# Performance work log

Hardware: AMD Instinct MI355X
Metric: run time of the kernel (lower is better)

Reference implementation:

```python
import jax, jax.numpy as jnp
import numpy as np
from jax import lax

L, H, NUM_CONVS, KSIZE = 8192, 128, 4, 7
EPS = 1e-5


def _pos_encoding(length, dim, dtype):
    pos = jnp.arange(length, dtype=jnp.float32)[:, None]
    i = jnp.arange(dim, dtype=jnp.float32)[None, :]
    angle = pos / jnp.power(10000.0, (2.0 * jnp.floor(i / 2.0)) / dim)
    pe = jnp.where((jnp.arange(dim) % 2 == 0)[None, :], jnp.sin(angle), jnp.cos(angle))
    return pe.astype(dtype)


def _layer_norm(x):
    mu = jnp.mean(x, axis=-1, keepdims=True)
    var = jnp.mean(jnp.square(x - mu), axis=-1, keepdims=True)
    return (x - mu) * lax.rsqrt(var + EPS)


def _conv1d_same(x, w, b):
    # x: [L, H]; w: [H_out, H_in, K]; b: [H_out]. SAME padding over sequence.
    lhs = x.T[None]  # [1, H, L]
    out = lax.conv_general_dilated(lhs, w, window_strides=(1,), padding='SAME',
                                   dimension_numbers=('NCH', 'OIH', 'NCH'))
    return (out[0] + b[:, None]).T  # [L, H]


def setup_inputs() -> dict:
    key = jax.random.key(0)
    ks = jax.random.split(key, 12)
    s = 0.02
    return {
        'x': jax.random.normal(ks[0], (L, H), jnp.float32),
        'conv_w': jax.random.normal(ks[1], (NUM_CONVS, H, H, KSIZE), jnp.float32) * s,
        'conv_b': jax.random.normal(ks[2], (NUM_CONVS, H), jnp.float32) * s,
        'Wq': jax.random.normal(ks[3], (H, H), jnp.float32) * s,
        'bq': jax.random.normal(ks[4], (H,), jnp.float32) * s,
        'Wk': jax.random.normal(ks[5], (H, H), jnp.float32) * s,
        'bk': jax.random.normal(ks[6], (H,), jnp.float32) * s,
        'Wv': jax.random.normal(ks[7], (H, H), jnp.float32) * s,
        'bv': jax.random.normal(ks[8], (H,), jnp.float32) * s,
        'Wff': jax.random.normal(ks[9], (H, H), jnp.float32) * s,
        'bff': jax.random.normal(ks[10], (H,), jnp.float32) * s,
    }


def reference(x, conv_w, conv_b, Wq, bq, Wk, bk, Wv, bv, Wff, bff):
    h = x + _pos_encoding(x.shape[0], x.shape[1], x.dtype)
    # conv stack: LN -> conv -> residual, repeated num_convs times
    for i in range(NUM_CONVS):
        residual = h
        h = _conv1d_same(_layer_norm(h), conv_w[i], conv_b[i]) + residual
    # self-attention (single-head as written in the source)
    residual = h
    n = _layer_norm(h)
    q = n @ Wq.T + bq
    k = n @ Wk.T + bk
    v = n @ Wv.T + bv
    scale = 1.0 / jnp.sqrt(jnp.asarray(H, h.dtype))
    attn = jax.nn.softmax((q @ k.T) * scale, axis=-1)  # [L, L]
    h = attn @ v + residual
    # feed-forward
    residual = h
    h = jax.nn.relu(_layer_norm(h) @ Wff.T + bff) + residual
    return h
```

## Files before the change

kernel.cpp:

```cpp
#include <hip/hip_runtime.h>

#define LL 8192
#define HH 128

typedef __attribute__((ext_vector_type(8))) short short8v;
typedef __attribute__((ext_vector_type(4))) short short4v;
typedef __attribute__((ext_vector_type(4))) float f32x4;

__device__ inline short f2bf(float f) {
    union { float f; unsigned u; } x; x.f = f;
    unsigned r = (x.u + 0x7fffu + ((x.u >> 16) & 1u)) >> 16;
    return (short)r;
}
__device__ inline float bf2f(short s) {
    union { unsigned u; float f; } x; x.u = ((unsigned)(unsigned short)s) << 16;
    return x.f;
}

__device__ inline short* sAp(short* base, int row, int col) {
    int byte = (row << 8) + (col << 1);
    byte ^= (row & 7) << 4;
    return (short*)((char*)base + byte);
}

__device__ inline short8v ln_pack8(const float* rowF, int l15) {
    const float4 a = *(const float4*)&rowF[l15 * 8];
    const float4 b = *(const float4*)&rowF[l15 * 8 + 4];
    float s  = (a.x + a.y) + (a.z + a.w) + (b.x + b.y) + (b.z + b.w);
    float s2 = a.x * a.x + a.y * a.y + a.z * a.z + a.w * a.w
             + b.x * b.x + b.y * b.y + b.z * b.z + b.w * b.w;
#pragma unroll
    for (int off = 1; off <= 8; off <<= 1) {
        s  += __shfl_xor(s,  off, 64);
        s2 += __shfl_xor(s2, off, 64);
    }
    float mu = s * (1.f / 128.f);
    float var = s2 * (1.f / 128.f) - mu * mu;
    float rstd = rsqrtf(var + 1e-5f);
    short8v r;
    r[0] = f2bf((a.x - mu) * rstd);
    r[1] = f2bf((a.y - mu) * rstd);
    r[2] = f2bf((a.z - mu) * rstd);
    r[3] = f2bf((a.w - mu) * rstd);
    r[4] = f2bf((b.x - mu) * rstd);
    r[5] = f2bf((b.y - mu) * rstd);
    r[6] = f2bf((b.z - mu) * rstd);
    r[7] = f2bf((b.w - mu) * rstd);
    return r;
}

__global__ __launch_bounds__(256) void repack_all(const float* __restrict__ x,
                                                  const float* __restrict__ w,
                                                  const float* __restrict__ Wq,
                                                  const float* __restrict__ Wk,
                                                  const float* __restrict__ Wv,
                                                  const float* __restrict__ bq,
                                                  const float* __restrict__ bk,
                                                  const float* __restrict__ bv,
                                                  const float* __restrict__ Wff,
                                                  short* __restrict__ wkb,
                                                  short* __restrict__ wqkvb,
                                                  float* __restrict__ b3,
                                                  short* __restrict__ wffb,
                                                  float* __restrict__ h0) {
    const float qs = 0.08838834764831845f;
    int idx = blockIdx.x * 256 + threadIdx.x;
    if (idx < 458752) {
        int k = idx % 7;
        int t = idx / 7;
        int i = t % HH; t /= HH;
        int o = t % HH;
        int lay = t / HH;
        wkb[((lay * 7 + k) * HH + o) * HH + i] = f2bf(w[idx]);
    } else {
        int j = idx - 458752;
        if (j < 49152) {
            int t = j >> 14, r = j & 16383;
            float v = (t == 0) ? Wq[r] * qs : (t == 1) ? Wk[r] : Wv[r];
            wqkvb[j] = f2bf(v);
        } else if (j < 49536) {
            int jj = j - 49152;
            b3[jj] = (jj < 128) ? bq[jj] * qs : (jj < 256) ? bk[jj - 128] : bv[jj - 256];
        } else if (j < 65920) {
            int jj = j - 49536;
            wffb[jj] = f2bf(Wff[jj]);
        } else {
            int p = j - 65920;
            if (p < 262144) {
                int g = p >> 5, c4 = (p & 31) << 2;
                float4 val = *(const float4*)&x[g * HH + c4];
                float fg = (float)g;
#pragma unroll
                for (int h = 0; h < 2; h++) {
                    int i0 = c4 + h * 2;
                    float e = (float)i0 / 128.f;
                    float ang = fg / powf(10000.f, e);
                    ((float*)&val)[h * 2]     += sinf(ang);
                    ((float*)&val)[h * 2 + 1] += cosf(ang);
                }
                *(float4*)&h0[g * HH + c4] = val;
            }
        }
    }
}

__global__ __launch_bounds__(256, 4) void conv4qkv_kernel(const float* __restrict__ h0,
                                                          const short* __restrict__ wkb,
                                                          const float* __restrict__ conv_b,
                                                          const short* __restrict__ wqkvb,
                                                          const float* __restrict__ b3,
                                                          float* __restrict__ hB,
                                                          short* __restrict__ qb,
                                                          short* __restrict__ kb,
                                                          short* __restrict__ vt) {
    __shared__ float sF[48][132];
    __shared__ short sA[54 * 128];
    short* sT = sA + 20 * 128;
    int tid = threadIdx.x;
    int w = tid >> 6, lane = tid & 63;
    int l15 = lane & 15, quad = lane >> 4;
    int m0 = blockIdx.x * 16;
    int c0 = w * 32;

    for (int idx = tid; idx < 48 * 32; idx += 256) {
        int r = idx >> 5, c4 = (idx & 31) << 2;
        int g = m0 - 16 + r;
        float4 val = make_float4(0.f, 0.f, 0.f, 0.f);
        if (g >= 0 && g < LL) val = *(const float4*)&h0[g * HH + c4];
        *(float4*)&sF[r][c4] = val;
    }
    for (int idx = tid; idx < 6 * 64; idx += 256) {
        int rr = idx >> 6, cc = idx & 63;
        int row = (rr < 3) ? rr : 48 + rr;
        ((unsigned*)sA)[row * 64 + cc] = 0u;
    }

    for (int lay = 0; lay < 4; lay++) {
        __syncthreads();
#pragma unroll
        for (int rr = 0; rr < 3; rr++) {
            int row = rr * 16 + w * 4 + quad;
            short8v pk = ln_pack8(&sF[row][0], l15);
            int g = m0 - 16 + row;
            if (g < 0 || g >= LL) pk = (short8v)(short)0;
            *(short8v*)sAp(sA, row + 3, l15 * 8) = pk;
        }
        __syncthreads();
        f32x4 acc[3][2];
#pragma unroll
        for (int mt = 0; mt < 3; mt++) { acc[mt][0] = (f32x4)(0.f); acc[mt][1] = (f32x4)(0.f); }
        const short* wl = wkb + lay * 7 * HH * HH;
        for (int k = 0; k < 7; k++) {
            const short* b0 = wl + (k * HH + c0 + l15) * HH;
            const short* b1 = b0 + 16 * HH;
#pragma unroll
            for (int ks = 0; ks < 4; ks++) {
                short8v bf0 = *(const short8v*)&b0[ks * 32 + quad * 8];
                short8v bf1 = *(const short8v*)&b1[ks * 32 + quad * 8];
#pragma unroll
                for (int mt = 0; mt < 3; mt++) {
                    short8v af = *(const short8v*)sAp(sA, mt * 16 + l15 + k, ks * 32 + quad * 8);
                    acc[mt][0] = __builtin_amdgcn_mfma_f32_16x16x32_bf16(af, bf0, acc[mt][0], 0, 0, 0);
                    acc[mt][1] = __builtin_amdgcn_mfma_f32_16x16x32_bf16(af, bf1, acc[mt][1], 0, 0, 0);
                }
            }
        }
        float bb0 = conv_b[lay * HH + c0 + l15], bb1 = conv_b[lay * HH + c0 + 16 + l15];
#pragma unroll
        for (int mt = 0; mt < 3; mt++)
#pragma unroll
            for (int r = 0; r < 4; r++) {
                int row = mt * 16 + quad * 4 + r;
                sF[row][c0 + l15]      += acc[mt][0][r] + bb0;
                sF[row][c0 + 16 + l15] += acc[mt][1][r] + bb1;
            }
    }
    __syncthreads();
    for (int idx = tid; idx < 16 * 32; idx += 256) {
        int r = idx >> 5, c4 = (idx & 31) << 2;
        *(float4*)&hB[(m0 + r) * HH + c4] = *(const float4*)&sF[16 + r][c4];
    }
    {
        int row = w * 4 + quad;
        *(short8v*)sAp(sA, row, l15 * 8) = ln_pack8(&sF[16 + row][0], l15);
    }
    __syncthreads();
    short8v af4[4];
#pragma unroll
    for (int ks = 0; ks < 4; ks++)
        af4[ks] = *(const short8v*)sAp(sA, l15, ks * 32 + quad * 8);

    for (int t = 0; t < 3; t++) {
        f32x4 acc0 = (f32x4)(0.f), acc1 = (f32x4)(0.f);
        const short* b0 = wqkvb + (t * 128 + c0 + l15) * HH;
        const short* b1 = b0 + 16 * HH;
#pragma unroll
        for (int ks = 0; ks < 4; ks++) {
            short8v bf0 = *(const short8v*)&b0[ks * 32 + quad * 8];
            short8v bf1 = *(const short8v*)&b1[ks * 32 + quad * 8];
            acc0 = __builtin_amdgcn_mfma_f32_16x16x32_bf16(af4[ks], bf0, acc0, 0, 0, 0);
            acc1 = __builtin_amdgcn_mfma_f32_16x16x32_bf16(af4[ks], bf1, acc1, 0, 0, 0);
        }
        float bb0 = b3[t * 128 + c0 + l15], bb1 = b3[t * 128 + c0 + 16 + l15];
        if (t < 2) {
            short* o = (t == 0) ? qb : kb;
#pragma unroll
            for (int r = 0; r < 4; r++) {
                int lr = m0 + quad * 4 + r;
                o[lr * HH + c0 + l15]      = f2bf(acc0[r] + bb0);
                o[lr * HH + c0 + 16 + l15] = f2bf(acc1[r] + bb1);
            }
        } else {
#pragma unroll
            for (int r = 0; r < 4; r++) {
                sT[(w * 32 + l15) * 17 + quad * 4 + r]      = f2bf(acc0[r] + bb0);
                sT[(w * 32 + 16 + l15) * 17 + quad * 4 + r] = f2bf(acc1[r] + bb1);
            }
            asm volatile("s_waitcnt lgkmcnt(0)" ::: "memory");
#pragma unroll
            for (int cc = 0; cc < 8; cc++) {
                int col = cc * 4 + quad;
                vt[(c0 + col) * LL + m0 + l15] = sT[(w * 32 + col) * 17 + l15];
            }
        }
    }
}

#define FBN 64

__global__ __launch_bounds__(256, 2) void flash_mfma_kernel(const short* __restrict__ qs,
                                                            const short* __restrict__ ksrc,
                                                            const short* __restrict__ vsrc,
                                                            short* __restrict__ PO,
                                                            float* __restrict__ Pl,
                                                            int segrows) {
    __shared__ short sK[16 * 64 * 8];
    __shared__ short sV[16 * 64 * 8];
    __shared__ short sP[4][32][72];

    const int tid = threadIdx.x;
    const int w = tid >> 6, lane = tid & 63;
    const int l15 = lane & 15, quad = lane >> 4;
    const int m0 = blockIdx.x * 128;
    const int seg = blockIdx.y;
    const int jbeg = seg * segrows;
    const int nchunk = segrows >> 6;

    const int vdt_base = (w >> 1);
    const int vks2 = w & 1;

    short8v qf[2][4];
#pragma unroll
    for (int mt = 0; mt < 2; mt++)
#pragma unroll
        for (int ks = 0; ks < 4; ks++)
            qf[mt][ks] = *(const short8v*)&qs[(m0 + w * 32 + mt * 16 + l15) * HH + ks * 32 + quad * 8];

    float l_r[2][4] = {{0.f, 0.f, 0.f, 0.f}, {0.f, 0.f, 0.f, 0.f}};
    f32x4 o_acc[2][8];
#pragma unroll
    for (int mt = 0; mt < 2; mt++)
#pragma unroll
        for (int dt = 0; dt < 8; dt++) o_acc[mt][dt] = (f32x4)(0.f);

    short8v kr[4], vr[4];
#pragma unroll
    for (int r = 0; r < 4; r++) {
        kr[r] = *(const short8v*)&ksrc[(jbeg + r * 16 + l15) * HH + w * 32 + quad * 8];
        vr[r] = *(const short8v*)&vsrc[((2 * r + vdt_base) * 16 + l15) * LL + jbeg + vks2 * 32 + quad * 8];
    }

    for (int c = 0; c < nchunk; c++) {
        __syncthreads();
#pragma unroll
        for (int r = 0; r < 4; r++) {
            *(short8v*)&sK[((w + 4 * r) * 64 + lane) * 8] = kr[r];
            *(short8v*)&sV[((w + 4 * r) * 64 + lane) * 8] = vr[r];
        }
        __syncthreads();
        if (c + 1 < nchunk) {
            const int j1 = jbeg + (c + 1) * FBN;
#pragma unroll
            for (int r = 0; r < 4; r++) {
                kr[r] = *(const short8v*)&ksrc[(j1 + r * 16 + l15) * HH + w * 32 + quad * 8];
                vr[r] = *(const short8v*)&vsrc[((2 * r + vdt_base) * 16 + l15) * LL + j1 + vks2 * 32 + quad * 8];
            }
        }
        f32x4 s_acc[2][4];
#pragma unroll
        for (int mt = 0; mt < 2; mt++)
#pragma unroll
            for (int nt = 0; nt < 4; nt++) s_acc[mt][nt] = (f32x4)(0.f);
#pragma unroll
        for (int nt = 0; nt < 4; nt++)
#pragma unroll
            for (int ks = 0; ks < 4; ks++) {
                short8v kf = *(const short8v*)&sK[((nt * 4 + ks) * 64 + lane) * 8];
                s_acc[0][nt] = __builtin_amdgcn_mfma_f32_16x16x32_bf16(qf[0][ks], kf, s_acc[0][nt], 0, 0, 0);
                s_acc[1][nt] = __builtin_amdgcn_mfma_f32_16x16x32_bf16(qf[1][ks], kf, s_acc[1][nt], 0, 0, 0);
            }
#pragma unroll
        for (int mt = 0; mt < 2; mt++)
#pragma unroll
            for (int nt = 0; nt < 4; nt++)
#pragma unroll
                for (int r = 0; r < 4; r++) {
                    float p = __expf(fminf(s_acc[mt][nt][r], 30.f));
                    l_r[mt][r] += p;
                    union { float f; unsigned u; } cv; cv.f = p;
                    sP[w][mt * 16 + quad * 4 + r][nt * 16 + l15] = (short)(cv.u >> 16);
                }
        asm volatile("s_waitcnt lgkmcnt(0)" ::: "memory");
#pragma unroll
        for (int ks2 = 0; ks2 < 2; ks2++) {
            short8v pf0 = *(const short8v*)&sP[w][l15][ks2 * 32 + quad * 8];
            short8v pf1 = *(const short8v*)&sP[w][16 + l15][ks2 * 32 + quad * 8];
#pragma unroll
            for (int dt = 0; dt < 8; dt++) {
                short8v vf = *(const short8v*)&sV[((dt * 2 + ks2) * 64 + lane) * 8];
                o_acc[0][dt] = __builtin_amdgcn_mfma_f32_16x16x32_bf16(pf0, vf, o_acc[0][dt], 0, 0, 0);
                o_acc[1][dt] = __builtin_amdgcn_mfma_f32_16x16x32_bf16(pf1, vf, o_acc[1][dt], 0, 0, 0);
            }
        }
    }
#pragma unroll
    for (int mt = 0; mt < 2; mt++)
#pragma unroll
        for (int r = 0; r < 4; r++) {
            float v = l_r[mt][r];
            v += __shfl_xor(v, 1, 64);
            v += __shfl_xor(v, 2, 64);
            v += __shfl_xor(v, 4, 64);
            v += __shfl_xor(v, 8, 64);
            if (l15 == 0)
                Pl[seg * LL + m0 + w * 32 + mt * 16 + quad * 4 + r] = v;
        }
#pragma unroll
    for (int mt = 0; mt < 2; mt++)
#pragma unroll
        for (int dt = 0; dt < 8; dt++)
#pragma unroll
            for (int r = 0; r < 4; r++)
                PO[(size_t)seg * LL * HH + (m0 + w * 32 + mt * 16 + quad * 4 + r) * HH + dt * 16 + l15] =
                    f2bf(o_acc[mt][dt][r]);
}

__global__ __launch_bounds__(256) void ff_kernel(const float* __restrict__ hin,
                                                 const short* __restrict__ PO,
                                                 const float* __restrict__ Pl,
                                                 const short* __restrict__ wffb,
                                                 const float* __restrict__ bff,
                                                 float* __restrict__ out,
                                                 int nsplit) {
    __shared__ float sF[16][132];
    __shared__ short sA[16 * 128];
    __shared__ float sLi[16];
    int tid = threadIdx.x;
    int w = tid >> 6, lane = tid & 63;
    int l15 = lane & 15, quad = lane >> 4;
    int m0 = blockIdx.x * 16;

    if (tid < 16) {
        float s = 0.f;
        for (int seg = 0; seg < nsplit; seg++) s += Pl[seg * LL + m0 + tid];
        sLi[tid] = 1.f / s;
    }
    __syncthreads();
    for (int idx = tid; idx < 16 * 32; idx += 256) {
        int r = idx >> 5, c4 = (idx & 31) << 2;
        float4 hv = *(const float4*)&hin[(m0 + r) * HH + c4];
        float s0 = 0.f, s1 = 0.f, s2 = 0.f, s3 = 0.f;
        for (int seg = 0; seg < nsplit; seg++) {
            short4v pv = *(const short4v*)&PO[(size_t)seg * LL * HH + (m0 + r) * HH + c4];
            s0 += bf2f(pv[0]); s1 += bf2f(pv[1]); s2 += bf2f(pv[2]); s3 += bf2f(pv[3]);
        }
        float li = sLi[r];
        *(float4*)&sF[r][c4] = make_float4(hv.x + s0 * li, hv.y + s1 * li,
                                           hv.z + s2 * li, hv.w + s3 * li);
    }
    __syncthreads();
    {
        int row = w * 4 + quad;
        *(short8v*)sAp(sA, row, l15 * 8) = ln_pack8(&sF[row][0], l15);
    }
    __syncthreads();
    int c0 = w * 32;
    f32x4 acc0 = (f32x4)(0.f), acc1 = (f32x4)(0.f);
    const short* b0 = wffb + (c0 + l15) * HH;
    const short* b1 = b0 + 16 * HH;
#pragma unroll
    for (int ks = 0; ks < 4; ks++) {
        short8v af = *(const short8v*)sAp(sA, l15, ks * 32 + quad * 8);
        short8v bf0 = *(const short8v*)&b0[ks * 32 + quad * 8];
        short8v bf1 = *(const short8v*)&b1[ks * 32 + quad * 8];
        acc0 = __builtin_amdgcn_mfma_f32_16x16x32_bf16(af, bf0, acc0, 0, 0, 0);
        acc1 = __builtin_amdgcn_mfma_f32_16x16x32_bf16(af, bf1, acc1, 0, 0, 0);
    }
    float bb0 = bff[c0 + l15], bb1 = bff[c0 + 16 + l15];
#pragma unroll
    for (int r = 0; r < 4; r++) {
        int lr = quad * 4 + r;
        out[(m0 + lr) * HH + c0 + l15]      = fmaxf(acc0[r] + bb0, 0.f) + sF[lr][c0 + l15];
        out[(m0 + lr) * HH + c0 + 16 + l15] = fmaxf(acc1[r] + bb1, 0.f) + sF[lr][c0 + 16 + l15];
    }
}

extern "C" void kernel_launch(void* const* d_in, const int* in_sizes, int n_in,
                              void* d_out, int out_size, void* d_ws, size_t ws_size,
                              hipStream_t stream) {
    const float* x      = (const float*)d_in[0];
    const float* conv_w = (const float*)d_in[1];
    const float* conv_b = (const float*)d_in[2];
    const float* Wq = (const float*)d_in[3];
    const float* bq = (const float*)d_in[4];
    const float* Wk = (const float*)d_in[5];
    const float* bk = (const float*)d_in[6];
    const float* Wv = (const float*)d_in[7];
    const float* bv = (const float*)d_in[8];
    const float* Wff = (const float*)d_in[9];
    const float* bff = (const float*)d_in[10];
    float* out = (float*)d_out;

    char* ws = (char*)d_ws;
    const size_t MB = 1u << 20;
    float* hB   = (float*)(ws);
    short* qb   = (short*)(ws + 4 * MB);
    short* kb   = (short*)(ws + 6 * MB);
    short* vt   = (short*)(ws + 8 * MB);
    float* Pl   = (float*)(ws + 10 * MB);
    short* wffb = (short*)(ws + 10 * MB + 524288);
    short* PO   = (short*)(ws + 10 * MB + 524288 + 32768);
    short* wkb   = (short*)(ws + 16 * MB);
    short* wqkvb = (short*)(ws + 17 * MB);
    float* b3    = (float*)(ws + 17 * MB + 131072);
    float* h0    = (float*)(ws + 18 * MB);

    int nsplit = (ws_size >= (size_t)44 * MB) ? 16 : 8;
    int segrows = LL / nsplit;

    repack_all<<<3074, 256, 0, stream>>>(x, conv_w, Wq, Wk, Wv, bq, bk, bv, Wff,
                                         wkb, wqkvb, b3, wffb, h0);
    conv4qkv_kernel<<<LL / 16, 256, 0, stream>>>(h0, wkb, conv_b, wqkvb, b3,
                                                 hB, qb, kb, vt);
    flash_mfma_kernel<<<dim3(LL / 128, nsplit), 256, 0, stream>>>(qb, kb, vt, PO, Pl, segrows);
    ff_kernel<<<LL / 16, 256, 0, stream>>>(hB, PO, Pl, wffb, bff, out, nsplit);
}
```

Before: 224.4 us.

## Split fused conv stack into per-layer kernels and separate QKV kernel

Replaces the fused conv4qkv kernel, which recomputed a 48-row halo window per 16-row tile to run all four conv layers in shared memory, with four per-layer conv launches that each need only a 3-row halo. Each layer round-trips through global memory, and the output columns are split across two blocks for more parallelism. QKV projection becomes its own kernel with a grid dimension per Q/K/V. This removes the roughly 3x redundant halo compute of the fused version. In exchange it adds extra launches and global memory traffic for the intermediate activations.

After: 229.6 us. 1.02x slower.

```diff
diff --git a/kernel.cpp b/kernel.cpp
--- a/kernel.cpp
+++ b/kernel.cpp
@@ -104,124 +104,112 @@
     }
 }
 
-__global__ __launch_bounds__(256, 4) void conv4qkv_kernel(const float* __restrict__ h0,
-                                                          const short* __restrict__ wkb,
-                                                          const float* __restrict__ conv_b,
-                                                          const short* __restrict__ wqkvb,
-                                                          const float* __restrict__ b3,
-                                                          float* __restrict__ hB,
-                                                          short* __restrict__ qb,
-                                                          short* __restrict__ kb,
-                                                          short* __restrict__ vt) {
-    __shared__ float sF[48][132];
-    __shared__ short sA[54 * 128];
-    short* sT = sA + 20 * 128;
+__global__ __launch_bounds__(256, 4) void conv_layer_kernel(const float* __restrict__ hin,
+                                                            const short* __restrict__ wkb,
+                                                            const float* __restrict__ conv_b,
+                                                            float* __restrict__ hout,
+                                                            int lay) {
+    __shared__ float sF[22][132];
+    __shared__ short sA[22 * 128];
+    int tid = threadIdx.x;
+    int w = tid >> 6, lane = tid & 63;
+    int l15 = lane & 15, quad = lane >> 4;
+    int m0 = (blockIdx.x >> 1) * 16;
+    int c0w = (blockIdx.x & 1) * 64 + w * 16;
+
+    for (int idx = tid; idx < 22 * 32; idx += 256) {
+        int r = idx >> 5, c4 = (idx & 31) << 2;
+        int g = m0 - 3 + r;
+        float4 val = make_float4(0.f, 0.f, 0.f, 0.f);
+        if (g >= 0 && g < LL) val = *(const float4*)&hin[g * HH + c4];
+        *(float4*)&sF[r][c4] = val;
+    }
+    __syncthreads();
+#pragma unroll
+    for (int rr = 0; rr < 2; rr++) {
+        int row = rr * 16 + w * 4 + quad;
+        if (row < 22)
+            *(short8v*)sAp(sA, row, l15 * 8) = ln_pack8(&sF[row][0], l15);
+    }
+    __syncthreads();
+    f32x4 accA = (f32x4)(0.f), accB = (f32x4)(0.f);
+    const short* wl = wkb + lay * 7 * HH * HH;
+    for (int k = 0; k < 7; k++) {
+        const short* b0 = wl + (k * HH + c0w + l15) * HH;
+#pragma unroll
+        for (int ks = 0; ks < 4; ks++) {
+            short8v bf = *(const short8v*)&b0[ks * 32 + quad * 8];
+            short8v af = *(const short8v*)sAp(sA, l15 + k, ks * 32 + quad * 8);
+            if (ks & 1) accB = __builtin_amdgcn_mfma_f32_16x16x32_bf16(af, bf, accB, 0, 0, 0);
+            else        accA = __builtin_amdgcn_mfma_f32_16x16x32_bf16(af, bf, accA, 0, 0, 0);
+        }
+    }
+    float bb = conv_b[lay * HH + c0w + l15];
+#pragma unroll
+    for (int r = 0; r < 4; r++) {
+        int row = quad * 4 + r;
+        hout[(m0 + row) * HH + c0w + l15] =
+            sF[3 + row][c0w + l15] + accA[r] + accB[r] + bb;
+    }
+}
+
+__global__ __launch_bounds__(256, 4) void qkv_kernel(const float* __restrict__ h4,
+                                                     const short* __restrict__ wqkvb,
+                                                     const float* __restrict__ b3,
+                                                     short* __restrict__ qb,
+                                                     short* __restrict__ kb,
+                                                     short* __restrict__ vt) {
+    __shared__ float sF[16][132];
+    __shared__ short sA[16 * 128];
+    __shared__ short sT[4][32][17];
     int tid = threadIdx.x;
     int w = tid >> 6, lane = tid & 63;
     int l15 = lane & 15, quad = lane >> 4;
     int m0 = blockIdx.x * 16;
-    int c0 = w * 32;
-
-    for (int idx = tid; idx < 48 * 32; idx += 256) {
-        int r = idx >> 5, c4 = (idx & 31) << 2;
-        int g = m0 - 16 + r;
-        float4 val = make_float4(0.f, 0.f, 0.f, 0.f);
-        if (g >= 0 && g < LL) val = *(const float4*)&h0[g * HH + c4];
-        *(float4*)&sF[r][c4] = val;
-    }
-    for (int idx = tid; idx < 6 * 64; idx += 256) {
-        int rr = idx >> 6, cc = idx & 63;
-        int row = (rr < 3) ? rr : 48 + rr;
-        ((unsigned*)sA)[row * 64 + cc] = 0u;
-    }
-
-    for (int lay = 0; lay < 4; lay++) {
-        __syncthreads();
-#pragma unroll
-        for (int rr = 0; rr < 3; rr++) {
-            int row = rr * 16 + w * 4 + quad;
-            short8v pk = ln_pack8(&sF[row][0], l15);
-            int g = m0 - 16 + row;
-            if (g < 0 || g >= LL) pk = (short8v)(short)0;
-            *(short8v*)sAp(sA, row + 3, l15 * 8) = pk;
-        }
-        __syncthreads();
-        f32x4 acc[3][2];
-#pragma unroll
-        for (int mt = 0; mt < 3; mt++) { acc[mt][0] = (f32x4)(0.f); acc[mt][1] = (f32x4)(0.f); }
-        const short* wl = wkb + lay * 7 * HH * HH;
-        for (int k = 0; k < 7; k++) {
-            const short* b0 = wl + (k * HH + c0 + l15) * HH;
-            const short* b1 = b0 + 16 * HH;
-#pragma unroll
-            for (int ks = 0; ks < 4; ks++) {
-                short8v bf0 = *(const short8v*)&b0[ks * 32 + quad * 8];
-                short8v bf1 = *(const short8v*)&b1[ks * 32 + quad * 8];
-#pragma unroll
-                for (int mt = 0; mt < 3; mt++) {
-                    short8v af = *(const short8v*)sAp(sA, mt * 16 + l15 + k, ks * 32 + quad * 8);
-                    acc[mt][0] = __builtin_amdgcn_mfma_f32_16x16x32_bf16(af, bf0, acc[mt][0], 0, 0, 0);
-                    acc[mt][1] = __builtin_amdgcn_mfma_f32_16x16x32_bf16(af, bf1, acc[mt][1], 0, 0, 0);
-                }
-            }
-        }
-        float bb0 = conv_b[lay * HH + c0 + l15], bb1 = conv_b[lay * HH + c0 + 16 + l15];
-#pragma unroll
-        for (int mt = 0; mt < 3; mt++)
-#pragma unroll
-            for (int r = 0; r < 4; r++) {
-                int row = mt * 16 + quad * 4 + r;
-                sF[row][c0 + l15]      += acc[mt][0][r] + bb0;
-                sF[row][c0 + 16 + l15] += acc[mt][1][r] + bb1;
-            }
-    }
-    __syncthreads();
+    int t = blockIdx.y;
+
     for (int idx = tid; idx < 16 * 32; idx += 256) {
         int r = idx >> 5, c4 = (idx & 31) << 2;
-        *(float4*)&hB[(m0 + r) * HH + c4] = *(const float4*)&sF[16 + r][c4];
-    }
+        *(float4*)&sF[r][c4] = *(const float4*)&h4[(m0 + r) * HH + c4];
+    }
+    __syncthreads();
     {
         int row = w * 4 + quad;
-        *(short8v*)sAp(sA, row, l15 * 8) = ln_pack8(&sF[16 + row][0], l15);
-    }
-    __syncthreads();
-    short8v af4[4];
-#pragma unroll
-    for (int ks = 0; ks < 4; ks++)
-        af4[ks] = *(const short8v*)sAp(sA, l15, ks * 32 + quad * 8);
-
-    for (int t = 0; t < 3; t++) {
-        f32x4 acc0 = (f32x4)(0.f), acc1 = (f32x4)(0.f);
-        const short* b0 = wqkvb + (t * 128 + c0 + l15) * HH;
-        const short* b1 = b0 + 16 * HH;
-#pragma unroll
-        for (int ks = 0; ks < 4; ks++) {
-            short8v bf0 = *(const short8v*)&b0[ks * 32 + quad * 8];
-            short8v bf1 = *(const short8v*)&b1[ks * 32 + quad * 8];
-            acc0 = __builtin_amdgcn_mfma_f32_16x16x32_bf16(af4[ks], bf0, acc0, 0, 0, 0);
-            acc1 = __builtin_amdgcn_mfma_f32_16x16x32_bf16(af4[ks], bf1, acc1, 0, 0, 0);
-        }
-        float bb0 = b3[t * 128 + c0 + l15], bb1 = b3[t * 128 + c0 + 16 + l15];
-        if (t < 2) {
-            short* o = (t == 0) ? qb : kb;
-#pragma unroll
-            for (int r = 0; r < 4; r++) {
-                int lr = m0 + quad * 4 + r;
-                o[lr * HH + c0 + l15]      = f2bf(acc0[r] + bb0);
-                o[lr * HH + c0 + 16 + l15] = f2bf(acc1[r] + bb1);
-            }
-        } else {
-#pragma unroll
-            for (int r = 0; r < 4; r++) {
-                sT[(w * 32 + l15) * 17 + quad * 4 + r]      = f2bf(acc0[r] + bb0);
-                sT[(w * 32 + 16 + l15) * 17 + quad * 4 + r] = f2bf(acc1[r] + bb1);
-            }
-            asm volatile("s_waitcnt lgkmcnt(0)" ::: "memory");
-#pragma unroll
-            for (int cc = 0; cc < 8; cc++) {
-                int col = cc * 4 + quad;
-                vt[(c0 + col) * LL + m0 + l15] = sT[(w * 32 + col) * 17 + l15];
-            }
+        *(short8v*)sAp(sA, row, l15 * 8) = ln_pack8(&sF[row][0], l15);
+    }
+    __syncthreads();
+    int c0 = w * 32;
+    f32x4 acc0 = (f32x4)(0.f), acc1 = (f32x4)(0.f);
+    const short* b0 = wqkvb + (t * 128 + c0 + l15) * HH;
+    const short* b1 = b0 + 16 * HH;
+#pragma unroll
+    for (int ks = 0; ks < 4; ks++) {
+        short8v af = *(const short8v*)sAp(sA, l15, ks * 32 + quad * 8);
+        short8v bf0 = *(const short8v*)&b0[ks * 32 + quad * 8];
+        short8v bf1 = *(const short8v*)&b1[ks * 32 + quad * 8];
+        acc0 = __builtin_amdgcn_mfma_f32_16x16x32_bf16(af, bf0, acc0, 0, 0, 0);
+        acc1 = __builtin_amdgcn_mfma_f32_16x16x32_bf16(af, bf1, acc1, 0, 0, 0);
+    }
+    float bb0 = b3[t * 128 + c0 + l15], bb1 = b3[t * 128 + c0 + 16 + l15];
+    if (t < 2) {
+        short* o = (t == 0) ? qb : kb;
+#pragma unroll
+        for (int r = 0; r < 4; r++) {
+            int lr = m0 + quad * 4 + r;
+            o[lr * HH + c0 + l15]      = f2bf(acc0[r] + bb0);
+            o[lr * HH + c0 + 16 + l15] = f2bf(acc1[r] + bb1);
+        }
+    } else {
+#pragma unroll
+        for (int r = 0; r < 4; r++) {
+            sT[w][l15][quad * 4 + r]      = f2bf(acc0[r] + bb0);
+            sT[w][16 + l15][quad * 4 + r] = f2bf(acc1[r] + bb1);
+        }
+        asm volatile("s_waitcnt lgkmcnt(0)" ::: "memory");
+#pragma unroll
+        for (int cc = 0; cc < 8; cc++) {
+            int col = cc * 4 + quad;
+            vt[(c0 + col) * LL + m0 + l15] = sT[w][col][l15];
         }
     }
 }
@@ -434,14 +422,19 @@
     short* wqkvb = (short*)(ws + 17 * MB);
     float* b3    = (float*)(ws + 17 * MB + 131072);
     float* h0    = (float*)(ws + 18 * MB);
+    float* h13   = (float*)(ws + 22 * MB);
+    float* h2    = h0;
 
     int nsplit = (ws_size >= (size_t)44 * MB) ? 16 : 8;
     int segrows = LL / nsplit;
 
     repack_all<<<3074, 256, 0, stream>>>(x, conv_w, Wq, Wk, Wv, bq, bk, bv, Wff,
                                          wkb, wqkvb, b3, wffb, h0);
-    conv4qkv_kernel<<<LL / 16, 256, 0, stream>>>(h0, wkb, conv_b, wqkvb, b3,
-                                                 hB, qb, kb, vt);
+    conv_layer_kernel<<<LL / 16 * 2, 256, 0, stream>>>(h0,  wkb, conv_b, h13, 0);
+    conv_layer_kernel<<<LL / 16 * 2, 256, 0, stream>>>(h13, wkb, conv_b, h2,  1);
+    conv_layer_kernel<<<LL / 16 * 2, 256, 0, stream>>>(h2,  wkb, conv_b, h13, 2);
+    conv_layer_kernel<<<LL / 16 * 2, 256, 0, stream>>>(h13, wkb, conv_b, hB,  3);
+    qkv_kernel<<<dim3(LL / 16, 3), 256, 0, stream>>>(hB, wqkvb, b3, qb, kb, vt);
     flash_mfma_kernel<<<dim3(LL / 128, nsplit), 256, 0, stream>>>(qb, kb, vt, PO, Pl, segrows);
     ff_kernel<<<LL / 16, 256, 0, stream>>>(hB, PO, Pl, wffb, bff, out, nsplit);
 }
```
